# Optimization experiments

Measured on AMD Instinct MI355X. Metric: run time of the kernel, lower is better.

The kernel has to match this reference:

```python
import jax, jax.numpy as jnp
import numpy as np

B, T = 8, 1024
IN_FEAT = 1024
N_FEAT = 1024
N_HEAD = 16
D_K = N_FEAT // N_HEAD
KERNEL = 11
LEFT_PAD = (KERNEL - 1) // 2  # sanm_shift=0
RIGHT_PAD = KERNEL - 1 - LEFT_PAD


def setup_inputs() -> dict:
    key = jax.random.key(0)
    ks = jax.random.split(key, 7)
    hidden_states = jax.random.normal(ks[0], (B, T, IN_FEAT), dtype=jnp.float32)
    mask = jax.random.randint(ks[1], (B, 1, T), 0, 2, dtype=jnp.int32)
    s_qkv = 1.0 / np.sqrt(IN_FEAT)
    s_out = 1.0 / np.sqrt(N_FEAT)
    W_qkv = jax.random.normal(ks[2], (3 * N_FEAT, IN_FEAT), dtype=jnp.float32) * s_qkv
    b_qkv = jnp.zeros((3 * N_FEAT,), dtype=jnp.float32)
    W_out = jax.random.normal(ks[3], (N_FEAT, N_FEAT), dtype=jnp.float32) * s_out
    b_out = jnp.zeros((N_FEAT,), dtype=jnp.float32)
    fsmn_kernel = jax.random.normal(ks[4], (N_FEAT, 1, KERNEL), dtype=jnp.float32) * (1.0 / KERNEL)
    return {"hidden_states": hidden_states, "mask": mask, "W_qkv": W_qkv,
            "b_qkv": b_qkv, "W_out": W_out, "b_out": b_out, "fsmn_kernel": fsmn_kernel}


def _fsmn(v, maskf, fsmn_kernel):
    # v: [B,T,D], maskf: [B,T,1]
    vm = v * maskf
    x = jnp.transpose(vm, (0, 2, 1))  # [B,D,T]
    x = jnp.pad(x, ((0, 0), (0, 0), (LEFT_PAD, RIGHT_PAD)))
    # depthwise conv1d (cross-correlation, matching torch Conv1d)
    y = jax.lax.conv_general_dilated(
        x, fsmn_kernel, window_strides=(1,), padding='VALID',
        dimension_numbers=('NCH', 'OIH', 'NCH'), feature_group_count=N_FEAT)
    y = jnp.transpose(y, (0, 2, 1)) + vm  # [B,T,D]
    return y * maskf


def reference(hidden_states, mask, W_qkv, b_qkv, W_out, b_out, fsmn_kernel):
    b, t, _ = hidden_states.shape
    qkv = jnp.einsum('btf,of->bto', hidden_states, W_qkv) + b_qkv  # [B,T,3*N_FEAT]
    q, k, v = jnp.split(qkv, 3, axis=-1)
    def heads(x):
        return jnp.transpose(x.reshape(b, t, N_HEAD, D_K), (0, 2, 1, 3))  # [B,H,T,D_K]
    q_h, k_h, v_h = heads(q), heads(k), heads(v)

    maskf = mask.reshape(b, t, 1).astype(hidden_states.dtype)
    fsmn_memory = _fsmn(v, maskf, fsmn_kernel)

    scale = D_K ** -0.5
    scores = jnp.einsum('bhqd,bhkd->bhqk', q_h * scale, k_h)  # [B,H,T,T]
    mask_keys = (mask.reshape(b, 1, 1, t) == 0)  # True where padded
    scores = jnp.where(mask_keys, -jnp.inf, scores)
    attn = jax.nn.softmax(scores, axis=-1)
    attn = jnp.where(mask_keys, 0.0, attn)
    ctx = jnp.einsum('bhqk,bhkd->bhqd', attn, v_h)  # [B,H,T,D_K]
    ctx = jnp.transpose(ctx, (0, 2, 1, 3)).reshape(b, t, N_FEAT)
    att_outs = jnp.einsum('btf,of->bto', ctx, W_out) + b_out
    return att_outs + fsmn_memory
```

## Files before the change

### kernel.cpp

```cpp
#include <hip/hip_runtime.h>
#include <stdint.h>


typedef uint16_t u16;
typedef float f32x4 __attribute__((ext_vector_type(4)));
typedef __bf16 bf16x8 __attribute__((ext_vector_type(8)));
typedef __bf16 bf16x2 __attribute__((ext_vector_type(2)));
typedef u16 u16x8 __attribute__((ext_vector_type(8)));
typedef u16 u16x4 __attribute__((ext_vector_type(4)));
typedef short s16x4 __attribute__((ext_vector_type(4)));

__device__ __forceinline__ u16 f2bf(float f) {
    union { float f; uint32_t u; } c; c.f = f;
    uint32_t u = c.u;
    return (u16)((u + 0x7fffu + ((u >> 16) & 1u)) >> 16);
}
__device__ __forceinline__ float bf2f(u16 h) {
    union { uint32_t u; float f; } c; c.u = ((uint32_t)h) << 16;
    return c.f;
}
__device__ __forceinline__ uint32_t pack_bf16(float a, float b) {
    bf16x2 t; t[0] = (__bf16)a; t[1] = (__bf16)b;
    union { bf16x2 v; uint32_t u; } c; c.v = t; return c.u;
}

__global__ __launch_bounds__(256) void cvt_f32_bf16(const float* __restrict__ src,
                                                    u16* __restrict__ dst, int n) {
    int i = (blockIdx.x * 256 + threadIdx.x) * 4;
    if (i >= n) return;
    float4 v = *reinterpret_cast<const float4*>(src + i);
    ushort4 o;
    o.x = f2bf(v.x); o.y = f2bf(v.y); o.z = f2bf(v.z); o.w = f2bf(v.w);
    *reinterpret_cast<ushort4*>(dst + i) = o;
}

__global__ void maskbits_kernel(const int* __restrict__ mask, uint32_t* __restrict__ mb) {
    int i = threadIdx.x;
    int b = i >> 5, c = i & 31;
    uint32_t u = 0;
    for (int j = 0; j < 32; ++j)
        u |= (mask[(b << 10) + c * 32 + j] ? 1u : 0u) << j;
    mb[i] = u;
}

__global__ __launch_bounds__(256) void fsmn_kt(const float* __restrict__ fk,
                                               float* __restrict__ kt) {
    int idx = blockIdx.x * 256 + threadIdx.x;
    if (idx < 11 * 1024) {
        int j = idx >> 10, c = idx & 1023;
        kt[idx] = fk[c * 11 + j];
    }
}

__global__ __launch_bounds__(256) void transpose_v(const u16* __restrict__ vn,
                                                   u16* __restrict__ vt) {
    __shared__ u16 ts[64][68];
    const int tid = threadIdx.x;
    const int bh = blockIdx.x >> 4;
    const int kc = blockIdx.x & 15;
    const u16* src = vn + ((size_t)bh << 16) + (size_t)kc * 64 * 64;
#pragma unroll
    for (int it = 0; it < 2; ++it) {
        int ch = it * 256 + tid;
        int k = ch >> 3, g = ch & 7;
        *reinterpret_cast<u16x8*>(&ts[k][g * 8]) =
            *reinterpret_cast<const u16x8*>(src + k * 64 + g * 8);
    }
    __syncthreads();
    u16* dst = vt + ((size_t)bh << 16) + kc * 64;
#pragma unroll
    for (int it = 0; it < 2; ++it) {
        int ch = it * 256 + tid;
        int d = ch >> 3, gk = ch & 7;
        u16x8 v;
#pragma unroll
        for (int j = 0; j < 8; ++j) v[j] = ts[gk * 8 + j][d];
        *reinterpret_cast<u16x8*>(dst + (size_t)d * 1024 + gk * 8) = v;
    }
}

template<int MODE>
__global__ __launch_bounds__(512, 4) void gemm_bk32(
    const u16* __restrict__ A, const u16* __restrict__ Bw, int M, int N, int K,
    int ntiles_n, const float* __restrict__ bias,
    u16* __restrict__ qo, u16* __restrict__ ko, u16* __restrict__ vo,
    float* __restrict__ out)
{
    __shared__ u16 lds[24576];
    const int t = threadIdx.x;
    const int lane = t & 63;
    const int wave = t >> 6;
    const int wr = wave >> 2, wc = wave & 3;
    const int lr = lane & 15, lq = lane >> 4;
    const int r3 = lane >> 2, c4 = lane & 3;
    const int cpx = gridDim.x >> 3;
    const int bid = (blockIdx.x & 7) * cpx + (blockIdx.x >> 3);
    const int m0 = (bid / ntiles_n) * 128;
    const int n0 = (bid % ntiles_n) * 256;
    const int NT = K >> 5;

    const u16* AgW  = A  + (size_t)(m0 + wave * 16 + r3) * K + c4 * 8;
    const u16* BgW0 = Bw + (size_t)(n0 + wave * 16 + r3) * K + c4 * 8;
    const u16* BgW1 = BgW0 + (size_t)128 * K;

    auto stage = [&](int buf, int tile) {
        u16* dA  = lds + buf * 12288 + wave * 512;
        u16* dB0 = lds + buf * 12288 + 4096 + wave * 512;
        u16* dB1 = dB0 + 4096;
        __builtin_amdgcn_global_load_lds(
            (const __attribute__((address_space(1))) void*)(AgW + tile * 32),
            (__attribute__((address_space(3))) void*)dA, 16, 0, 0);
        __builtin_amdgcn_global_load_lds(
            (const __attribute__((address_space(1))) void*)(BgW0 + tile * 32),
            (__attribute__((address_space(3))) void*)dB0, 16, 0, 0);
        __builtin_amdgcn_global_load_lds(
            (const __attribute__((address_space(1))) void*)(BgW1 + tile * 32),
            (__attribute__((address_space(3))) void*)dB1, 16, 0, 0);
    };

    f32x4 acc[4][4];
#pragma unroll
    for (int i = 0; i < 4; ++i)
#pragma unroll
        for (int j = 0; j < 4; ++j) acc[i][j] = (f32x4){0.f, 0.f, 0.f, 0.f};

    stage(0, 0);
    asm volatile("s_waitcnt vmcnt(0)" ::: "memory");
    __builtin_amdgcn_s_barrier();

    for (int T = 0; T < NT; ++T) {
        const int p = T & 1;
        const u16* Ab = lds + p * 12288;
        const u16* Bb = Ab + 4096;
        bf16x8 a[4], bb[4];
#pragma unroll
        for (int mm = 0; mm < 4; ++mm)
            a[mm] = *reinterpret_cast<const bf16x8*>(Ab + (wr * 64 + mm * 16 + lr) * 32 + lq * 8);
#pragma unroll
        for (int nn = 0; nn < 4; ++nn)
            bb[nn] = *reinterpret_cast<const bf16x8*>(Bb + (wc * 64 + nn * 16 + lr) * 32 + lq * 8);
        if (T + 1 < NT) stage(p ^ 1, T + 1);
        __builtin_amdgcn_s_setprio(1);
#pragma unroll
        for (int mm = 0; mm < 4; ++mm)
#pragma unroll
            for (int nn = 0; nn < 4; ++nn)
                acc[mm][nn] = __builtin_amdgcn_mfma_f32_16x16x32_bf16(a[mm], bb[nn], acc[mm][nn], 0, 0, 0);
        __builtin_amdgcn_s_setprio(0);
        if (T + 1 < NT) asm volatile("s_waitcnt vmcnt(0)" ::: "memory");
        __builtin_amdgcn_s_barrier();
    }

#pragma unroll
    for (int m = 0; m < 4; ++m) {
        int row = m0 + wr * 64 + m * 16 + lq * 4;
#pragma unroll
        for (int n = 0; n < 4; ++n) {
            int col = n0 + wc * 64 + n * 16 + lr;
            float bv = bias[col];
#pragma unroll
            for (int r = 0; r < 4; ++r) {
                float val = acc[m][n][r] + bv;
                int rr = row + r;
                if (MODE == 0) {
                    int part = col >> 10;
                    int cc = col & 1023;
                    int h = cc >> 6, d = cc & 63;
                    int b = rr >> 10, tt = rr & 1023;
                    size_t bh = (size_t)(b * 16 + h);
                    u16* dst = (part == 0) ? qo : (part == 1) ? ko : vo;
                    dst[((bh << 10) + tt) * 64 + d] = f2bf(part == 0 ? val * 0.18033688011f : val);
                } else {
                    size_t o = (size_t)rr * N + col;
                    out[o] += val;
                }
            }
        }
    }
}

__global__ __launch_bounds__(256) void fsmn_v3(const u16* __restrict__ vt,
                                               const int* __restrict__ mask,
                                               const float* __restrict__ kt,
                                               float* __restrict__ out)
{
    __shared__ float vs[64][147];
    __shared__ float ms[144];
    const int tid = threadIdx.x;
    const int tc = blockIdx.x & 7;
    const int bh = blockIdx.x >> 3;
    const int b = bh >> 4, h = bh & 15;
    const int t0 = tc * 128;
    const u16* vrow = vt + ((size_t)bh << 16);
    const int* mrow = mask + (b << 10);

    if (tid < 144) {
        int tt = t0 - 8 + tid;
        ms[tid] = (tt >= 0 && tt < 1024) ? (float)mrow[tt] : 0.f;
    }
    const int sd = tid >> 2;
    const int ci0 = tid & 3;
#pragma unroll
    for (int it = 0; it < 5; ++it) {
        int ci = ci0 + it * 4;
        if (ci < 18) {
            int tbase = t0 - 8 + ci * 8;
            if (tbase >= 0 && tbase < 1024) {
                u16x8 v8 = *reinterpret_cast<const u16x8*>(vrow + (size_t)sd * 1024 + tbase);
#pragma unroll
                for (int j = 0; j < 8; ++j)
                    vs[sd][ci * 8 + j] = bf2f((u16)v8[j]) * (float)mrow[tbase + j];
            } else {
#pragma unroll
                for (int j = 0; j < 8; ++j) vs[sd][ci * 8 + j] = 0.f;
            }
        }
    }
    __syncthreads();

    const int dd = tid & 63;
    const int tg = tid >> 6;
    const int c = h * 64 + dd;
    float kc[11];
#pragma unroll
    for (int j = 0; j < 11; ++j) kc[j] = kt[j * 1024 + c];

    const int tl0 = tg * 32;
    float w[11];
#pragma unroll
    for (int j = 0; j < 11; ++j) w[j] = vs[dd][3 + tl0 + j];
    float* orow = out + ((size_t)(b * 1024 + t0 + tl0)) * 1024 + c;
#pragma unroll 4
    for (int s = 0; s < 32; ++s) {
        float acc = 0.f;
#pragma unroll
        for (int j = 0; j < 11; ++j) acc += kc[j] * w[j];
        float mf = ms[8 + tl0 + s];
        orow[(size_t)s * 1024] = (acc + w[5]) * mf;
#pragma unroll
        for (int j = 0; j < 10; ++j) w[j] = w[j + 1];
        w[10] = vs[dd][3 + tl0 + s + 11];
    }
}

__global__ __launch_bounds__(256) void attn_v6(const u16* __restrict__ qg,
                                               const u16* __restrict__ kg,
                                               const u16* __restrict__ vtg,
                                               const uint32_t* __restrict__ mbits,
                                               u16* __restrict__ ctx)
{
    __shared__ u16 K_s[2][64 * 64];
    __shared__ u16 V_s[2][64 * 64];
    const int t = threadIdx.x;
    const int lane = t & 63;
    const int w = t >> 6;
    const int lr = lane & 15, lq = lane >> 4;
    const int bh = blockIdx.x & 127;
    const int qc = blockIdx.x >> 7;
    const int b = bh >> 4, h = bh & 15;
    const size_t base = (size_t)bh << 16;
    const u16* kb = kg + base;
    const u16* vb = vtg + base;
    const int q0 = qc * 128 + w * 32;

    bf16x8 qf[2][2];
#pragma unroll
    for (int qt = 0; qt < 2; ++qt)
#pragma unroll
        for (int kk = 0; kk < 2; ++kk)
            qf[qt][kk] = *reinterpret_cast<const bf16x8*>(
                qg + base + (size_t)(q0 + qt * 16 + lr) * 64 + kk * 32 + lq * 8);

    f32x4 oacc[2][4];
    float l_[2] = {0.f, 0.f};
#pragma unroll
    for (int qt = 0; qt < 2; ++qt)
#pragma unroll
        for (int dt = 0; dt < 4; ++dt) oacc[qt][dt] = (f32x4){0.f, 0.f, 0.f, 0.f};

    const uint32_t* mrow = mbits + b * 32;

    auto stage = [&](int bufi, int tile) {
        const int k0s = tile * 64;
#pragma unroll
        for (int rd = 0; rd < 2; ++rd) {
            int ch = rd * 256 + w * 64 + lane;
            int row = ch >> 3, c7 = ch & 7;
            int sc = (c7 ^ (row & 7)) * 8;
            const u16* srcK = kb + (size_t)(k0s + row) * 64 + sc;
            const u16* srcV = vb + (size_t)row * 1024 + k0s + sc;
            u16* dK = &K_s[bufi][(size_t)(rd * 256 + w * 64) * 8];
            u16* dV = &V_s[bufi][(size_t)(rd * 256 + w * 64) * 8];
            __builtin_amdgcn_global_load_lds(
                (const __attribute__((address_space(1))) void*)srcK,
                (__attribute__((address_space(3))) void*)dK, 16, 0, 0);
            __builtin_amdgcn_global_load_lds(
                (const __attribute__((address_space(1))) void*)srcV,
                (__attribute__((address_space(3))) void*)dV, 16, 0, 0);
        }
    };

    int cur = 0;
    stage(0, 0);
    asm volatile("s_waitcnt vmcnt(0)");
    __syncthreads();

    for (int it = 0; it < 16; ++it) {
        if (it < 15) stage(cur ^ 1, it + 1);

        const u16* Kb = K_s[cur];
        bf16x8 kf[4][2];
#pragma unroll
        for (int kt = 0; kt < 4; ++kt) {
            int row = kt * 16 + lr;
#pragma unroll
            for (int kk = 0; kk < 2; ++kk) {
                int g = (kk * 4 + lq) ^ (row & 7);
                kf[kt][kk] = *reinterpret_cast<const bf16x8*>(Kb + row * 64 + g * 8);
            }
        }

        f32x4 s[2][4];
#pragma unroll
        for (int qt = 0; qt < 2; ++qt)
#pragma unroll
            for (int kt = 0; kt < 4; ++kt) {
                f32x4 acc = (f32x4){0.f, 0.f, 0.f, 0.f};
                acc = __builtin_amdgcn_mfma_f32_16x16x32_bf16(kf[kt][0], qf[qt][0], acc, 0, 0, 0);
                acc = __builtin_amdgcn_mfma_f32_16x16x32_bf16(kf[kt][1], qf[qt][1], acc, 0, 0, 0);
                s[qt][kt] = acc;
            }

        const uint32_t mw0 = mrow[it * 2], mw1 = mrow[it * 2 + 1];
        uint32_t mb_[4];
        mb_[0] = mw0 >> (lq * 4);
        mb_[1] = mw0 >> (16 + lq * 4);
        mb_[2] = mw1 >> (lq * 4);
        mb_[3] = mw1 >> (16 + lq * 4);

        const u16* Vb = V_s[cur];
        s16x4 vf[4][4];
#pragma unroll
        for (int ks = 0; ks < 4; ++ks)
#pragma unroll
            for (int dt = 0; dt < 4; ++dt) {
                int row = dt * 16 + lr;
                int g = (ks * 2 + (lq >> 1)) ^ (row & 7);
                vf[ks][dt] = *reinterpret_cast<const s16x4*>(Vb + row * 64 + g * 8 + (lq & 1) * 4);
            }

#pragma unroll
        for (int qt = 0; qt < 2; ++qt) {
            float p[4][4], rs = 0.f;
#pragma unroll
            for (int kt = 0; kt < 4; ++kt)
#pragma unroll
                for (int r = 0; r < 4; ++r) {
                    float pv = __builtin_amdgcn_exp2f(s[qt][kt][r]);
                    pv = (mb_[kt] & (1u << r)) ? pv : 0.f;
                    p[kt][r] = pv;
                    rs += pv;
                }
            rs += __shfl_xor(rs, 16, 64);
            rs += __shfl_xor(rs, 32, 64);
            l_[qt] += rs;

            union { uint32_t u[2]; s16x4 v; } pa[4];
#pragma unroll
            for (int kt = 0; kt < 4; ++kt) {
                pa[kt].u[0] = pack_bf16(p[kt][0], p[kt][1]);
                pa[kt].u[1] = pack_bf16(p[kt][2], p[kt][3]);
            }

#pragma unroll
            for (int dt = 0; dt < 4; ++dt) {
                f32x4 o = oacc[qt][dt];
#pragma unroll
                for (int kt = 0; kt < 4; ++kt)
                    o = __builtin_amdgcn_mfma_f32_16x16x16bf16_1k(vf[kt][dt], pa[kt].v, o, 0, 0, 0);
                oacc[qt][dt] = o;
            }
        }

        asm volatile("s_waitcnt vmcnt(0)" ::: "memory");
        __syncthreads();
        cur ^= 1;
    }

#pragma unroll
    for (int qt = 0; qt < 2; ++qt) {
        float li = 1.f / l_[qt];
        int trow = q0 + qt * 16 + lr;
        u16* crow = ctx + ((size_t)(b << 10) + trow) * 1024 + h * 64;
#pragma unroll
        for (int dt = 0; dt < 4; ++dt) {
            f32x4 o = oacc[qt][dt];
            u16x4 pkv;
            pkv[0] = f2bf(o[0] * li); pkv[1] = f2bf(o[1] * li);
            pkv[2] = f2bf(o[2] * li); pkv[3] = f2bf(o[3] * li);
            *reinterpret_cast<u16x4*>(crow + dt * 16 + lq * 4) = pkv;
        }
    }
}

extern "C" void kernel_launch(void* const* d_in, const int* in_sizes, int n_in,
                              void* d_out, int out_size, void* d_ws, size_t ws_size,
                              hipStream_t stream)
{
    (void)in_sizes; (void)n_in; (void)out_size; (void)ws_size;
    const float* hs   = (const float*)d_in[0];
    const int*   mask = (const int*)d_in[1];
    const float* Wqkv = (const float*)d_in[2];
    const float* bqkv = (const float*)d_in[3];
    const float* Wout = (const float*)d_in[4];
    const float* bout = (const float*)d_in[5];
    const float* fk   = (const float*)d_in[6];
    float* out = (float*)d_out;

    char* ws = (char*)d_ws;
    u16* hsb   = (u16*)(ws);
    u16* wqkvb = (u16*)(ws + 16777216);
    u16* woutb = (u16*)(ws + 23068672);
    u16* qb    = (u16*)(ws + 25165824);
    u16* kb    = (u16*)(ws + 41943040);
    u16* vtb   = (u16*)(ws + 58720256);
    u16* vnb   = (u16*)(ws + 75497472);
    u16* ctxb  = (u16*)(ws + 75497472);
    uint32_t* mbits = (uint32_t*)ws;
    float* ktT = (float*)(ws + 4096);

    cvt_f32_bf16<<<8192, 256, 0, stream>>>(hs,   hsb,   8388608);
    cvt_f32_bf16<<<3072, 256, 0, stream>>>(Wqkv, wqkvb, 3145728);
    cvt_f32_bf16<<<1024, 256, 0, stream>>>(Wout, woutb, 1048576);

    gemm_bk32<0><<<64 * 12, 512, 0, stream>>>(hsb, wqkvb, 8192, 3072, 1024, 12,
                                              bqkv, qb, kb, vnb, nullptr);
    maskbits_kernel<<<1, 256, 0, stream>>>(mask, mbits);
    fsmn_kt<<<44, 256, 0, stream>>>(fk, ktT);
    transpose_v<<<2048, 256, 0, stream>>>(vnb, vtb);
    fsmn_v3<<<1024, 256, 0, stream>>>(vtb, mask, ktT, out);
    attn_v6<<<1024, 256, 0, stream>>>(qb, kb, vtb, mbits, ctxb);
    gemm_bk32<1><<<64 * 4, 512, 0, stream>>>(ctxb, woutb, 8192, 1024, 1024, 4,
                                             bout, nullptr, nullptr, nullptr, out);
}
```

Baseline: 208.0 us.

## Fold mask into MFMA accumulator and compute row sums with ones-MFMA

The attention kernel now seeds the QK MFMA accumulator with a per-key mask bias of 0 or -3e38, so masked scores become zero after exp2 with no select. The softmax denominator comes from an extra MFMA that multiplies the bf16 probabilities by a vector of ones, replacing the VALU adds and cross-lane shuffles. The QK MFMAs move inside the per-query-tile loop and both MFMA phases are wrapped in s_setprio. The risk is that the row sum now uses bf16-rounded probabilities, which could shift numerics slightly, and there are four more MFMAs per tile.

```diff
diff --git a/kernel.cpp b/kernel.cpp
--- a/kernel.cpp
+++ b/kernel.cpp
@@ -243,7 +243,7 @@
     }
 }
 
-__global__ __launch_bounds__(256) void attn_v6(const u16* __restrict__ qg,
+__global__ __launch_bounds__(256) void attn_v7(const u16* __restrict__ qg,
                                                const u16* __restrict__ kg,
                                                const u16* __restrict__ vtg,
                                                const uint32_t* __restrict__ mbits,
@@ -272,11 +272,17 @@
                 qg + base + (size_t)(q0 + qt * 16 + lr) * 64 + kk * 32 + lq * 8);
 
     f32x4 oacc[2][4];
-    float l_[2] = {0.f, 0.f};
-#pragma unroll
-    for (int qt = 0; qt < 2; ++qt)
+    f32x4 oacc_l[2];
+#pragma unroll
+    for (int qt = 0; qt < 2; ++qt) {
+        oacc_l[qt] = (f32x4){0.f, 0.f, 0.f, 0.f};
 #pragma unroll
         for (int dt = 0; dt < 4; ++dt) oacc[qt][dt] = (f32x4){0.f, 0.f, 0.f, 0.f};
+    }
+
+    s16x4 ones_f;
+#pragma unroll
+    for (int j = 0; j < 4; ++j) ones_f[j] = (short)0x3F80;
 
     const uint32_t* mrow = mbits + b * 32;
 
@@ -320,23 +326,18 @@
             }
         }
 
-        f32x4 s[2][4];
-#pragma unroll
-        for (int qt = 0; qt < 2; ++qt)
-#pragma unroll
-            for (int kt = 0; kt < 4; ++kt) {
-                f32x4 acc = (f32x4){0.f, 0.f, 0.f, 0.f};
-                acc = __builtin_amdgcn_mfma_f32_16x16x32_bf16(kf[kt][0], qf[qt][0], acc, 0, 0, 0);
-                acc = __builtin_amdgcn_mfma_f32_16x16x32_bf16(kf[kt][1], qf[qt][1], acc, 0, 0, 0);
-                s[qt][kt] = acc;
-            }
-
         const uint32_t mw0 = mrow[it * 2], mw1 = mrow[it * 2 + 1];
         uint32_t mb_[4];
         mb_[0] = mw0 >> (lq * 4);
         mb_[1] = mw0 >> (16 + lq * 4);
         mb_[2] = mw1 >> (lq * 4);
         mb_[3] = mw1 >> (16 + lq * 4);
+        f32x4 ma[4];
+#pragma unroll
+        for (int kt = 0; kt < 4; ++kt)
+#pragma unroll
+            for (int r = 0; r < 4; ++r)
+                ma[kt][r] = (mb_[kt] & (1u << r)) ? 0.f : -3e38f;
 
         const u16* Vb = V_s[cur];
         s16x4 vf[4][4];
@@ -351,27 +352,27 @@
 
 #pragma unroll
         for (int qt = 0; qt < 2; ++qt) {
-            float p[4][4], rs = 0.f;
-#pragma unroll
-            for (int kt = 0; kt < 4; ++kt)
-#pragma unroll
-                for (int r = 0; r < 4; ++r) {
-                    float pv = __builtin_amdgcn_exp2f(s[qt][kt][r]);
-                    pv = (mb_[kt] & (1u << r)) ? pv : 0.f;
-                    p[kt][r] = pv;
-                    rs += pv;
-                }
-            rs += __shfl_xor(rs, 16, 64);
-            rs += __shfl_xor(rs, 32, 64);
-            l_[qt] += rs;
+            f32x4 s[4];
+            __builtin_amdgcn_s_setprio(1);
+#pragma unroll
+            for (int kt = 0; kt < 4; ++kt) {
+                s[kt] = __builtin_amdgcn_mfma_f32_16x16x32_bf16(kf[kt][0], qf[qt][0], ma[kt], 0, 0, 0);
+                s[kt] = __builtin_amdgcn_mfma_f32_16x16x32_bf16(kf[kt][1], qf[qt][1], s[kt], 0, 0, 0);
+            }
+            __builtin_amdgcn_s_setprio(0);
 
             union { uint32_t u[2]; s16x4 v; } pa[4];
 #pragma unroll
             for (int kt = 0; kt < 4; ++kt) {
-                pa[kt].u[0] = pack_bf16(p[kt][0], p[kt][1]);
-                pa[kt].u[1] = pack_bf16(p[kt][2], p[kt][3]);
-            }
-
+                float p0 = __builtin_amdgcn_exp2f(s[kt][0]);
+                float p1 = __builtin_amdgcn_exp2f(s[kt][1]);
+                float p2 = __builtin_amdgcn_exp2f(s[kt][2]);
+                float p3 = __builtin_amdgcn_exp2f(s[kt][3]);
+                pa[kt].u[0] = pack_bf16(p0, p1);
+                pa[kt].u[1] = pack_bf16(p2, p3);
+            }
+
+            __builtin_amdgcn_s_setprio(1);
 #pragma unroll
             for (int dt = 0; dt < 4; ++dt) {
                 f32x4 o = oacc[qt][dt];
@@ -380,6 +381,10 @@
                     o = __builtin_amdgcn_mfma_f32_16x16x16bf16_1k(vf[kt][dt], pa[kt].v, o, 0, 0, 0);
                 oacc[qt][dt] = o;
             }
+#pragma unroll
+            for (int kt = 0; kt < 4; ++kt)
+                oacc_l[qt] = __builtin_amdgcn_mfma_f32_16x16x16bf16_1k(ones_f, pa[kt].v, oacc_l[qt], 0, 0, 0);
+            __builtin_amdgcn_s_setprio(0);
         }
 
         asm volatile("s_waitcnt vmcnt(0)" ::: "memory");
@@ -389,7 +394,7 @@
 
 #pragma unroll
     for (int qt = 0; qt < 2; ++qt) {
-        float li = 1.f / l_[qt];
+        float li = 1.f / oacc_l[qt][0];
         int trow = q0 + qt * 16 + lr;
         u16* crow = ctx + ((size_t)(b << 10) + trow) * 1024 + h * 64;
 #pragma unroll
@@ -439,7 +444,7 @@
     fsmn_kt<<<44, 256, 0, stream>>>(fk, ktT);
     transpose_v<<<2048, 256, 0, stream>>>(vnb, vtb);
     fsmn_v3<<<1024, 256, 0, stream>>>(vtb, mask, ktT, out);
-    attn_v6<<<1024, 256, 0, stream>>>(qb, kb, vtb, mbits, ctxb);
+    attn_v7<<<1024, 256, 0, stream>>>(qb, kb, vtb, mbits, ctxb);
     gemm_bk32<1><<<64 * 4, 512, 0, stream>>>(ctxb, woutb, 8192, 1024, 1024, 4,
                                              bout, nullptr, nullptr, nullptr, out);
 }
```

Result: no change. 206.1 us (-0.9%).
